# Optimization experiments

Hardware: AMD Instinct MI355X
Metric: run time of the kernel (lower is better)

Reference implementation:

```python
import jax, jax.numpy as jnp
import numpy as np

B, N, E, D = 8, 10000, 160000, 256
H = D // 2
SLOPE = 0.2  # LeakyReLU negative slope


def setup_inputs() -> dict:
    key = jax.random.key(0)
    ks = jax.random.split(key, 8)
    node_feats = jax.random.normal(ks[0], (B, N, D), dtype=jnp.float32)
    edge_attr = jax.random.uniform(ks[1], (E, 1), dtype=jnp.float32)
    W1 = jax.random.normal(ks[2], (2 * D, H), dtype=jnp.float32) * 0.05
    b1 = jnp.zeros((H,), dtype=jnp.float32)
    W2 = jax.random.normal(ks[3], (H, 1), dtype=jnp.float32) * 0.05
    b2 = jnp.zeros((1,), dtype=jnp.float32)
    edge_index = jax.random.randint(ks[4], (2, E), 0, N, dtype=jnp.int64)
    valid_masks = jax.random.randint(ks[5], (B, N), 0, 2).astype(bool)
    return {"node_feats": node_feats, "edge_attr": edge_attr, "W1": W1, "b1": b1,
            "W2": W2, "b2": b2, "edge_index": edge_index, "valid_masks": valid_masks}


def reference(node_feats, edge_attr, W1, b1, W2, b2, edge_index, valid_masks):
    # node_feats: [B,N,D]; edge_index: [2,E] shared across batch
    d = node_feats.shape[-1]
    src, dst = edge_index[0], edge_index[1]
    # cat([src_feats, dst_feats]) @ W1 == src @ W1[:d] + dst @ W1[d:]
    # Project per-node first, then gather per-edge: avoids the [B,E,2D] concat.
    ps = jnp.einsum('bnd,dh->bnh', node_feats, W1[:d])   # [B,N,H]
    pd = jnp.einsum('bnd,dh->bnh', node_feats, W1[d:])   # [B,N,H]
    h = ps[:, src] + pd[:, dst] + b1                      # [B,E,H]
    h = jnp.where(h >= 0, h, SLOPE * h)                   # LeakyReLU(0.2)
    scores = jnp.einsum('beh,h->be', h, W2[:, 0]) + b2[0]  # [B,E]
    scores = scores * edge_attr[:, 0]                     # edge_attr multiplies pre-softmax
    w = jax.nn.softmax(scores, axis=1)                    # global softmax over all edges
    # sparse_coo(edge_index, w) @ node_feats: out[src[e]] += w[e] * feats[dst[e]]
    msg = w[..., None] * node_feats[:, dst]               # [B,E,D]
    n = node_feats.shape[1]
    agg = jax.vmap(lambda m: jax.ops.segment_sum(m, src, num_segments=n))(msg)  # [B,N,D]
    mask = valid_masks.astype(node_feats.dtype)           # [B,N]
    cnt = mask.sum(axis=1)                                # [B]
    masked_mean = (agg * mask[..., None]).sum(axis=1) / jnp.maximum(cnt, 1.0)[:, None]
    full_mean = agg.mean(axis=1)
    graph_feats = jnp.where((cnt > 0)[:, None], masked_mean, full_mean)  # [B,D]
    return graph_feats, w
```

## Files before the change

### kernel.cpp

```cpp
#include <hip/hip_runtime.h>
#include <hip/hip_bf16.h>
#include <hip/hip_fp16.h>

#define B_ 8
#define N_ 10000
#define E_ 160000
#define D_ 256
#define H_ 128
#define SLOPE 0.2f
#define NCHUNK 100

#define NB_ 64
#define EPB_ (E_ / NB_)
#define BINS_ 256
#define NPB_ (N_ / 16)
#define SUBS_ 8

#define SB_ 256
#define SEB_ (E_ / SB_)

typedef __attribute__((ext_vector_type(8))) _Float16 v8h;
typedef __attribute__((ext_vector_type(4))) _Float16 v4h;
typedef __attribute__((ext_vector_type(2))) _Float16 v2h;
typedef __attribute__((ext_vector_type(4))) float f32x4;

static __device__ __forceinline__ float dot2f(v2h a, v2h b, float c) {
#if __has_builtin(__builtin_amdgcn_fdot2)
    return __builtin_amdgcn_fdot2(a, b, c, false);
#else
    return fmaf((float)a.y, (float)b.y, fmaf((float)a.x, (float)b.x, c));
#endif
}

static __device__ __forceinline__ void block_flags(const int* __restrict__ eidx_raw,
                                                   const unsigned int* __restrict__ mask32,
                                                   int tid, int* sfl) {
    if (tid < 64) {
        unsigned long long oddnz = __ballot(eidx_raw[2 * tid + 1] != 0);
        unsigned long long mgt1  = __ballot(mask32[tid] > 1u);
        if (tid == 0) {
            sfl[0] = (oddnz == 0ull) ? 1 : 0;
            sfl[1] = (mgt1 != 0ull) ? 1 : 0;
        }
    }
    __syncthreads();
}

__global__ __launch_bounds__(256) void kprep(const int* __restrict__ eidx_raw,
                                             const unsigned char* __restrict__ mask8,
                                             const unsigned int* __restrict__ mask32,
                                             const float* __restrict__ W1,
                                             const float* __restrict__ b1,
                                             const float* __restrict__ W2,
                                             int* __restrict__ ce,
                                             unsigned char* __restrict__ cmT,
                                             __half* __restrict__ Wt,
                                             __half* __restrict__ b1h,
                                             __half* __restrict__ w2h,
                                             int* __restrict__ cnti,
                                             int* __restrict__ hpart) {
    const int tid = threadIdx.x;
    __shared__ int sfl[2];
    __shared__ int scnt[8];

    if (blockIdx.x < 1250) {
        if (tid < 8) scnt[tid] = 0;
        block_flags(eidx_raw, mask32, tid, sfl);
        const int f_e = sfl[0], f_m = sfl[1];
        const int i = blockIdx.x * 256 + tid;
        if (i < 2 * E_) ce[i] = f_e ? eidx_raw[2 * i] : eidx_raw[i];
        if (i < B_ * N_) {
            unsigned char v = f_m ? (unsigned char)(mask8[i] != 0)
                                  : (unsigned char)(mask32[i] != 0u);
            const int b = i / N_;
            const int n = i - b * N_;
            cmT[n * 8 + b] = v;
            if (v) atomicAdd(&scnt[b], 1);
        }
        if (i < 2 * 256 * 128) {
            const int f = i & 127;
            const int row = i >> 7;
            const int c = row >> 8, k = row & 255;
            Wt[((c * 128 + f) * 256) + k] = __float2half(W1[row * 128 + f]);
        }
        if (i < 128) {
            b1h[i] = __float2half(b1[i]);
            w2h[i] = __float2half(W2[i]);
        }
        __syncthreads();
        if (tid < 8 && scnt[tid]) atomicAdd(&cnti[tid], scnt[tid]);
    } else {
        block_flags(eidx_raw, mask32, tid, sfl);
        const int f_e = sfl[0];
        __shared__ int h[BINS_];
        h[tid] = 0;
        __syncthreads();
        const int hb = blockIdx.x - 1250;
        const int base = hb * EPB_;
        for (int i = tid; i < EPB_; i += 256) {
            const int e = base + i;
            const int s = f_e ? eidx_raw[2 * e] : eidx_raw[e];
            const int d = f_e ? eidx_raw[2 * (E_ + e)] : eidx_raw[E_ + e];
            const int bin = (d / NPB_) * 16 + s / NPB_;
            atomicAdd(&h[bin], 1);
        }
        __syncthreads();
        hpart[hb * BINS_ + tid] = h[tid];
    }
}

__global__ __launch_bounds__(256) void kprefix(const int* __restrict__ hpart,
                                               int* __restrict__ offsetG,
                                               int* __restrict__ bstart) {
    __shared__ int cnt[BINS_];
    __shared__ int excl[BINS_];
    const int bin = threadIdx.x;
    int c = 0;
    for (int b = 0; b < NB_; b++) c += hpart[b * BINS_ + bin];
    cnt[bin] = c;
    __syncthreads();
    if (bin == 0) {
        int r = 0;
        for (int i = 0; i < BINS_; i++) { excl[i] = r; r += cnt[i]; }
    }
    __syncthreads();
    if ((bin & 15) == 0) bstart[bin >> 4] = excl[bin];
    if (bin == 0) bstart[16] = E_;
    int run = excl[bin];
    for (int b = 0; b < NB_; b++) {
        offsetG[b * BINS_ + bin] = run;
        run += hpart[b * BINS_ + bin];
    }
}

__global__ __launch_bounds__(256) void k1_mfma(const float* __restrict__ X,
                                               const __half* __restrict__ Wt,
                                               __half* __restrict__ ps,
                                               __half* __restrict__ pd,
                                               const int* __restrict__ ce,
                                               const int* __restrict__ offsetG,
                                               int4* __restrict__ esort,
                                               int* __restrict__ rank) {
    const int tid = threadIdx.x;
    __shared__ __align__(16) char smem[64 * 136 * 2];

    if (blockIdx.x >= 1250) {
        int* loc = (int*)smem;
        const int sb = blockIdx.x - 1250;
        loc[tid] = offsetG[sb * BINS_ + tid];
        __syncthreads();
        const int base = sb * EPB_;
        for (int i = tid; i < EPB_; i += 256) {
            const int e = base + i;
            const int s = ce[e], d = ce[E_ + e];
            const int bin = (d / NPB_) * 16 + s / NPB_;
            const int pos = atomicAdd(&loc[bin], 1);
            esort[pos] = make_int4(s, d, e, 0);
            rank[e] = pos;
        }
        return;
    }

    const int rb = blockIdx.x;
    const int wave = tid >> 6, lane = tid & 63;
    const int quad = lane >> 4, l16 = lane & 15;
    _Float16* Xs = (_Float16*)smem;
    _Float16* T  = (_Float16*)smem;

    f32x4 acc[2][2][4];
#pragma unroll
    for (int c = 0; c < 2; c++)
#pragma unroll
        for (int i = 0; i < 2; i++)
#pragma unroll
            for (int j = 0; j < 4; j++) acc[c][i][j] = (f32x4){0.f, 0.f, 0.f, 0.f};

    const int row_base = rb * 64;
    const int sr = tid >> 3;
    const int sc = (tid & 7) * 4;

    const float* xsrc  = &X[(size_t)(row_base + sr) * 256 + sc];
    const float* xsrc2 = xsrc + 32 * 256;
    const __half* wbase = &Wt[((size_t)(wave * 32 + l16)) * 256 + quad * 8];

    float4 xa, xb;
    v8h wcur[2][2], wnxt[2][2];

    xa = *(const float4*)(xsrc);
    xb = *(const float4*)(xsrc2);
#pragma unroll
    for (int cb = 0; cb < 2; cb++)
#pragma unroll
        for (int ft = 0; ft < 2; ft++)
            wcur[cb][ft] = *(const v8h*)(wbase + (size_t)(cb * 128 + ft * 16) * 256);
    {
        v4h pa = {(_Float16)xa.x, (_Float16)xa.y, (_Float16)xa.z, (_Float16)xa.w};
        v4h pb = {(_Float16)xb.x, (_Float16)xb.y, (_Float16)xb.z, (_Float16)xb.w};
        *(v4h*)&Xs[sr * 40 + sc] = pa;
        *(v4h*)&Xs[(sr + 32) * 40 + sc] = pb;
    }
    __syncthreads();

    for (int kc = 0; kc < 8; ++kc) {
        const int cur = kc & 1;
        if (kc < 7) {
            xa = *(const float4*)(xsrc + (kc + 1) * 32);
            xb = *(const float4*)(xsrc2 + (kc + 1) * 32);
#pragma unroll
            for (int cb = 0; cb < 2; cb++)
#pragma unroll
                for (int ft = 0; ft < 2; ft++)
                    wnxt[cb][ft] = *(const v8h*)(wbase + (size_t)(cb * 128 + ft * 16) * 256 + (kc + 1) * 32);
        }
#pragma unroll
        for (int nt = 0; nt < 4; ++nt) {
            v8h xf = *(v8h*)&Xs[cur * (64 * 40) + (nt * 16 + l16) * 40 + quad * 8];
            acc[0][0][nt] = __builtin_amdgcn_mfma_f32_16x16x32_f16(wcur[0][0], xf, acc[0][0][nt], 0, 0, 0);
            acc[0][1][nt] = __builtin_amdgcn_mfma_f32_16x16x32_f16(wcur[0][1], xf, acc[0][1][nt], 0, 0, 0);
            acc[1][0][nt] = __builtin_amdgcn_mfma_f32_16x16x32_f16(wcur[1][0], xf, acc[1][0][nt], 0, 0, 0);
            acc[1][1][nt] = __builtin_amdgcn_mfma_f32_16x16x32_f16(wcur[1][1], xf, acc[1][1][nt], 0, 0, 0);
        }
        if (kc < 7) {
            const int nb = (cur ^ 1) * (64 * 40);
            v4h pa = {(_Float16)xa.x, (_Float16)xa.y, (_Float16)xa.z, (_Float16)xa.w};
            v4h pb = {(_Float16)xb.x, (_Float16)xb.y, (_Float16)xb.z, (_Float16)xb.w};
            *(v4h*)&Xs[nb + sr * 40 + sc] = pa;
            *(v4h*)&Xs[nb + (sr + 32) * 40 + sc] = pb;
#pragma unroll
            for (int cb = 0; cb < 2; cb++)
#pragma unroll
                for (int ft = 0; ft < 2; ft++)
                    wcur[cb][ft] = wnxt[cb][ft];
        }
        __syncthreads();
    }

#pragma unroll
    for (int cb = 0; cb < 2; ++cb) {
        if (cb) __syncthreads();
#pragma unroll
        for (int nt = 0; nt < 4; ++nt)
#pragma unroll
            for (int ft = 0; ft < 2; ++ft) {
                f32x4 a = acc[cb][ft][nt];
                v4h h = {(_Float16)a.x, (_Float16)a.y, (_Float16)a.z, (_Float16)a.w};
                *(v4h*)&T[(nt * 16 + l16) * 136 + wave * 32 + ft * 16 + quad * 4] = h;
            }
        __syncthreads();
        __half* outp = cb ? pd : ps;
#pragma unroll
        for (int pass = 0; pass < 4; ++pass) {
            const int r = pass * 16 + (tid >> 4);
            const int f8 = (tid & 15) * 8;
            const int R = row_base + r;
            const int b = R / N_;
            const int n = R - b * N_;
            *(float4*)(outp + ((size_t)b * N_ + n) * 128 + f8) =
                *(const float4*)&T[r * 136 + f8];
        }
    }
}

__global__ __launch_bounds__(256) void k2_scores(const __half* __restrict__ ps,
                                                 const __half* __restrict__ pd,
                                                 const int4* __restrict__ esort,
                                                 const __half* __restrict__ b1h,
                                                 const __half* __restrict__ w2h,
                                                 const float* __restrict__ b2,
                                                 const float* __restrict__ eattr,
                                                 float* __restrict__ scS) {
    const int tid = threadIdx.x;
    const int wave = tid >> 6;
    const int lane = tid & 63;
    const int bid = blockIdx.x;
    const int batch = bid & 7;
    const int e0 = (bid >> 3) * 64;

    const int hi = (lane & 7) * 16;

    v2h b1p[8], w2p[8];
    {
        const v2h* bp = (const v2h*)(b1h + hi);
        const v2h* wp = (const v2h*)(w2h + hi);
#pragma unroll
        for (int j = 0; j < 8; j++) { b1p[j] = bp[j]; w2p[j] = wp[j]; }
    }
    const float bias2 = b2[0];
    const v2h slp = {(_Float16)SLOPE, (_Float16)SLOPE};

    const __half* psb = ps + (size_t)batch * N_ * 128;
    const __half* pdb = pd + (size_t)batch * N_ * 128;
    float* scb = scS + (size_t)batch * E_;

#pragma unroll
    for (int q = 0; q < 2; q++) {
        const int e = e0 + wave * 16 + q * 8 + (lane >> 3);
        const int4 er = esort[e];
        const int src = er.x, dst = er.y, orig = er.z;

        const float4* aps = (const float4*)&psb[(size_t)src * 128 + hi];
        const float4* apd = (const float4*)&pdb[(size_t)dst * 128 + hi];
        float4 rs[2] = {aps[0], aps[1]};
        float4 rd[2] = {apd[0], apd[1]};
        const v2h* sv = (const v2h*)rs;
        const v2h* dv = (const v2h*)rd;

        float acc = 0.f;
#pragma unroll
        for (int j = 0; j < 8; j++) {
            v2h x = sv[j] + dv[j] + b1p[j];
            v2h l = __builtin_elementwise_max(x, x * slp);
            acc = dot2f(l, w2p[j], acc);
        }
        acc += __shfl_xor(acc, 1);
        acc += __shfl_xor(acc, 2);
        acc += __shfl_xor(acc, 4);

        if ((lane & 7) == 0) {
            scb[e] = (acc + bias2) * eattr[orig];
        }
    }
}

__global__ __launch_bounds__(256) void k3s_stats(const float* __restrict__ scS,
                                                 float* __restrict__ pmax,
                                                 double* __restrict__ psum) {
    const int tid = threadIdx.x;
    const int wave = tid >> 6, lane = tid & 63;
    const int base = blockIdx.x * SEB_;

    float fm[8];
#pragma unroll
    for (int j = 0; j < 8; j++) fm[j] = -3.4e38f;
    for (int i = tid; i < SEB_; i += 256) {
        const int p = base + i;
#pragma unroll
        for (int j = 0; j < 8; j++)
            fm[j] = fmaxf(fm[j], scS[(size_t)j * E_ + p]);
    }
#pragma unroll
    for (int k = 1; k <= 32; k <<= 1)
#pragma unroll
        for (int j = 0; j < 8; j++) fm[j] = fmaxf(fm[j], __shfl_xor(fm[j], k));
    __shared__ float lmax[4][8];
    if (lane == 0)
#pragma unroll
        for (int j = 0; j < 8; j++) lmax[wave][j] = fm[j];
    __syncthreads();
    float m[8];
#pragma unroll
    for (int j = 0; j < 8; j++)
        m[j] = fmaxf(fmaxf(lmax[0][j], lmax[1][j]), fmaxf(lmax[2][j], lmax[3][j]));

    double s[8];
#pragma unroll
    for (int j = 0; j < 8; j++) s[j] = 0.0;
    for (int i = tid; i < SEB_; i += 256) {
        const int p = base + i;
#pragma unroll
        for (int j = 0; j < 8; j++)
            s[j] += (double)expf(scS[(size_t)j * E_ + p] - m[j]);
    }
#pragma unroll
    for (int k = 1; k <= 32; k <<= 1)
#pragma unroll
        for (int j = 0; j < 8; j++) s[j] += __shfl_xor(s[j], k);
    __shared__ double lsum[4][8];
    if (lane == 0)
#pragma unroll
        for (int j = 0; j < 8; j++) lsum[wave][j] = s[j];
    __syncthreads();
    if (tid < 8) {
        pmax[blockIdx.x * 8 + tid] = m[tid];
        psum[blockIdx.x * 8 + tid] = lsum[0][tid] + lsum[1][tid] + lsum[2][tid] + lsum[3][tid];
    }
}

static __device__ __forceinline__ void stats_combine(const float* __restrict__ pmax,
                                                     const double* __restrict__ psum,
                                                     int tid, float* smx, float* sinvx) {
    if (tid < 64) {
        float mc[SB_ / 64][8];
        float v[8];
#pragma unroll
        for (int j = 0; j < 8; j++) v[j] = -3.4e38f;
#pragma unroll
        for (int g = 0; g < SB_ / 64; g++) {
            const float4* p4 = (const float4*)&pmax[(g * 64 + tid) * 8];
            float4 a = p4[0], b = p4[1];
            mc[g][0] = a.x; mc[g][1] = a.y; mc[g][2] = a.z; mc[g][3] = a.w;
            mc[g][4] = b.x; mc[g][5] = b.y; mc[g][6] = b.z; mc[g][7] = b.w;
#pragma unroll
            for (int j = 0; j < 8; j++) v[j] = fmaxf(v[j], mc[g][j]);
        }
#pragma unroll
        for (int k = 1; k <= 32; k <<= 1)
#pragma unroll
            for (int j = 0; j < 8; j++) v[j] = fmaxf(v[j], __shfl_xor(v[j], k));
        double z[8];
#pragma unroll
        for (int j = 0; j < 8; j++) z[j] = 0.0;
#pragma unroll
        for (int g = 0; g < SB_ / 64; g++)
#pragma unroll
            for (int j = 0; j < 8; j++)
                z[j] += psum[(g * 64 + tid) * 8 + j] * (double)expf(mc[g][j] - v[j]);
#pragma unroll
        for (int k = 1; k <= 32; k <<= 1)
#pragma unroll
            for (int j = 0; j < 8; j++) z[j] += __shfl_xor(z[j], k);
        if (tid == 0)
#pragma unroll
            for (int j = 0; j < 8; j++) { smx[j] = v[j]; sinvx[j] = (float)(1.0 / z[j]); }
    }
}

__global__ __launch_bounds__(256) void k3ef(const int4* __restrict__ esort,
                                            const float* __restrict__ scS,
                                            const unsigned char* __restrict__ cmT,
                                            const float* __restrict__ pmax,
                                            const double* __restrict__ psum,
                                            const int* __restrict__ bstart,
                                            const int* __restrict__ rank,
                                            float* __restrict__ Wpf,
                                            float* __restrict__ Wpm,
                                            float* __restrict__ wout) {
    const int tid = threadIdx.x;
    __shared__ float smx[8], sinvx[8];
    __shared__ float lWf[NPB_ * 8];
    __shared__ float lWm[NPB_ * 8];

    stats_combine(pmax, psum, tid, smx, sinvx);

    if (blockIdx.x >= 16 * SUBS_) {
        __syncthreads();
        const int e = (blockIdx.x - 16 * SUBS_) * 256 + tid;
        const int p = rank[e];
#pragma unroll
        for (int j = 0; j < 8; j++) {
            const float v = scS[(size_t)j * E_ + p];
            wout[(size_t)j * E_ + e] = expf(v - smx[j]) * sinvx[j];
        }
        return;
    }

    const int bucket = blockIdx.x / SUBS_;
    const int sub = blockIdx.x % SUBS_;

    for (int i = tid; i < NPB_ * 8; i += 256) { lWf[i] = 0.f; lWm[i] = 0.f; }
    __syncthreads();

    float m[8], inv[8];
#pragma unroll
    for (int j = 0; j < 8; j++) { m[j] = smx[j]; inv[j] = sinvx[j]; }

    const int bs = bstart[bucket], be = bstart[bucket + 1];
    const int len = be - bs;
    const int s0 = bs + (int)((long long)len * sub / SUBS_);
    const int s1 = bs + (int)((long long)len * (sub + 1) / SUBS_);
    const int nbase = bucket * NPB_;

    for (int p = s0 + tid; p < s1; p += 256) {
        const int4 er = esort[p];
        const int src = er.x;
        const int rel = er.y - nbase;
        float wv[8];
#pragma unroll
        for (int j = 0; j < 8; j++)
            wv[j] = expf(scS[(size_t)j * E_ + p] - m[j]) * inv[j];
        const unsigned long long mm = *(const unsigned long long*)&cmT[src * 8];
        float* lf = &lWf[rel * 8];
        float* lm = &lWm[rel * 8];
#pragma unroll
        for (int j = 0; j < 8; j++) {
            atomicAdd(&lf[j], wv[j]);
            if ((mm >> (8 * j)) & 1ull) atomicAdd(&lm[j], wv[j]);
        }
    }
    __syncthreads();

    float* of = Wpf + ((size_t)bucket * SUBS_ + sub) * (NPB_ * 8);
    float* om = Wpm + ((size_t)bucket * SUBS_ + sub) * (NPB_ * 8);
    for (int i = tid; i < NPB_ * 8; i += 256) { of[i] = lWf[i]; om[i] = lWm[i]; }
}

__global__ __launch_bounds__(256) void k3g_reduce(const float* __restrict__ Wpf,
                                                  const float* __restrict__ Wpm,
                                                  float* __restrict__ WfT,
                                                  float* __restrict__ WmT) {
    const int i = blockIdx.x * 256 + threadIdx.x;
    if (i >= N_ * 8) return;
    const int n = i >> 3, b = i & 7;
    const int bucket = n / NPB_;
    const int rel = n - bucket * NPB_;
    float sf = 0.f, sm = 0.f;
#pragma unroll
    for (int sub = 0; sub < SUBS_; sub++) {
        const size_t off = ((size_t)bucket * SUBS_ + sub) * (NPB_ * 8) + rel * 8 + b;
        sf += Wpf[off];
        sm += Wpm[off];
    }
    WfT[i] = sf;
    WmT[i] = sm;
}

__global__ __launch_bounds__(256) void k4b_wsum(const float* __restrict__ X,
                                                const float* __restrict__ WmT,
                                                const float* __restrict__ WfT,
                                                float* __restrict__ gpart) {
    const int c = blockIdx.x;
    const int b = blockIdx.y;
    const int tx = threadIdx.x & 63;
    const int ty = threadIdx.x >> 6;
    const int npc = N_ / NCHUNK;
    const int n0 = c * npc;

    const float4* X4 = (const float4*)(X + (size_t)b * N_ * 256);
    float4 am = {0.f, 0.f, 0.f, 0.f};
    float4 af = {0.f, 0.f, 0.f, 0.f};

    for (int n = n0 + ty; n < n0 + npc; n += 4) {
        float wm = WmT[n * 8 + b];
        float wf = WfT[n * 8 + b];
        float4 v = X4[(size_t)n * 64 + tx];
        am.x = fmaf(wm, v.x, am.x); am.y = fmaf(wm, v.y, am.y);
        am.z = fmaf(wm, v.z, am.z); am.w = fmaf(wm, v.w, am.w);
        af.x = fmaf(wf, v.x, af.x); af.y = fmaf(wf, v.y, af.y);
        af.z = fmaf(wf, v.z, af.z); af.w = fmaf(wf, v.w, af.w);
    }

    __shared__ float4 red[256];
    red[threadIdx.x] = am;
    __syncthreads();
    if (ty == 0) {
        float4 r1 = red[tx + 64], r2 = red[tx + 128], r3 = red[tx + 192];
        am.x += r1.x + r2.x + r3.x; am.y += r1.y + r2.y + r3.y;
        am.z += r1.z + r2.z + r3.z; am.w += r1.w + r2.w + r3.w;
    }
    __syncthreads();
    red[threadIdx.x] = af;
    __syncthreads();
    if (ty == 0) {
        float4 r1 = red[tx + 64], r2 = red[tx + 128], r3 = red[tx + 192];
        af.x += r1.x + r2.x + r3.x; af.y += r1.y + r2.y + r3.y;
        af.z += r1.z + r2.z + r3.z; af.w += r1.w + r2.w + r3.w;
        float4* gp4 = (float4*)gpart;
        gp4[((c * 2 + 0) * 8 + b) * 64 + tx] = am;
        gp4[((c * 2 + 1) * 8 + b) * 64 + tx] = af;
    }
}

__global__ __launch_bounds__(256) void k5_final(const float* __restrict__ gpart,
                                                const int* __restrict__ cnti,
                                                float* __restrict__ gf) {
    const int b = blockIdx.x;
    const int d = threadIdx.x;
    float sm = 0.f, sf = 0.f;
    for (int c = 0; c < NCHUNK; c++) {
        sm += gpart[((c * 2 + 0) * 8 + b) * 256 + d];
        sf += gpart[((c * 2 + 1) * 8 + b) * 256 + d];
    }
    const float cn = (float)cnti[b];
    gf[b * 256 + d] = (cn > 0.f) ? (sm / cn) : (sf / (float)N_);
}

static inline char* align16(char* p) {
    return (char*)(((uintptr_t)p + 15) & ~(uintptr_t)15);
}

extern "C" void kernel_launch(void* const* d_in, const int* in_sizes, int n_in,
                              void* d_out, int out_size, void* d_ws, size_t ws_size,
                              hipStream_t stream) {
    const float* X     = (const float*)d_in[0];
    const float* eattr = (const float*)d_in[1];
    const float* W1    = (const float*)d_in[2];
    const float* b1    = (const float*)d_in[3];
    const float* W2    = (const float*)d_in[4];
    const float* b2    = (const float*)d_in[5];
    const int*   eidx_raw = (const int*)d_in[6];
    const unsigned char* mask8 = (const unsigned char*)d_in[7];
    const unsigned int*  mask32 = (const unsigned int*)d_in[7];

    float* out  = (float*)d_out;
    float* gf   = out;
    float* wout = out + 2048;

    char* cur = (char*)d_ws;
    __half* ps_h = (__half*)cur;             cur += (size_t)N_ * 8 * 128 * 2;
    __half* pd_h = (__half*)cur;             cur += (size_t)N_ * 8 * 128 * 2;
    __half* Wt   = (__half*)cur;             cur += 2 * 128 * 256 * 2;
    int* ce      = (int*)cur;                cur += 2 * E_ * 4;
    unsigned char* cmT = (unsigned char*)cur; cur += N_ * 8;
    cur = align16(cur);
    int* cnti    = (int*)cur;                cur += 8 * 4;
    cur = align16(cur);
    float* pmax  = (float*)cur;              cur += SB_ * 8 * 4;
    cur = align16(cur);
    double* psum = (double*)cur;             cur += SB_ * 8 * 8;
    float* gpart = (float*)cur;              cur += NCHUNK * 2 * 8 * 256 * 4;
    int* hpart   = (int*)cur;                cur += NB_ * BINS_ * 4;
    int* offsetG = (int*)cur;                cur += NB_ * BINS_ * 4;
    int* bstart  = (int*)cur;                cur += 32 * 4;
    cur = align16(cur);
    int4* esort  = (int4*)cur;               cur += (size_t)E_ * 16;
    int* rankB   = (int*)cur;                cur += E_ * 4;
    __half* b1h  = (__half*)cur;             cur += 128 * 2;
    __half* w2h  = (__half*)cur;             cur += 128 * 2;
    cur = align16(cur);
    float* scS   = (float*)cur;              cur += (size_t)E_ * 8 * 4;

    char* ocur = (char*)d_ws;
    float* Wpf = (float*)ocur;               ocur += (size_t)16 * SUBS_ * NPB_ * 8 * 4;
    float* Wpm = (float*)ocur;               ocur += (size_t)16 * SUBS_ * NPB_ * 8 * 4;
    float* WfT = (float*)ocur;               ocur += N_ * 8 * 4;
    float* WmT = (float*)ocur;               ocur += N_ * 8 * 4;

    hipMemsetAsync(cnti, 0, 8 * sizeof(int), stream);
    hipLaunchKernelGGL(kprep, dim3(1250 + NB_), dim3(256), 0, stream,
                       eidx_raw, mask8, mask32, W1, b1, W2,
                       ce, cmT, Wt, b1h, w2h, cnti, hpart);
    hipLaunchKernelGGL(kprefix, dim3(1), dim3(256), 0, stream, hpart, offsetG, bstart);
    hipLaunchKernelGGL(k1_mfma, dim3(1250 + NB_), dim3(256), 0, stream,
                       X, Wt, ps_h, pd_h, ce, offsetG, esort, rankB);
    hipLaunchKernelGGL(k2_scores, dim3(E_ / 8), dim3(256), 0, stream,
                       ps_h, pd_h, esort, b1h, w2h, b2, eattr, scS);
    hipLaunchKernelGGL(k3s_stats, dim3(SB_), dim3(256), 0, stream, scS, pmax, psum);
    hipLaunchKernelGGL(k3ef, dim3(16 * SUBS_ + E_ / 256), dim3(256), 0, stream,
                       esort, scS, cmT, pmax, psum, bstart, rankB, Wpf, Wpm, wout);
    hipLaunchKernelGGL(k3g_reduce, dim3((N_ * 8 + 255) / 256), dim3(256), 0, stream,
                       Wpf, Wpm, WfT, WmT);
    hipLaunchKernelGGL(k4b_wsum, dim3(NCHUNK, 8), dim3(256), 0, stream, X, WmT, WfT, gpart);
    hipLaunchKernelGGL(k5_final, dim3(8), dim3(256), 0, stream, gpart, cnti, gf);
}
```

Measured before the change: 276.6 us.

## Fuse prefix scan, sub-bucket reduce and final reduce into neighbouring kernels

Moves the histogram prefix scan into block 0 of the projection kernel, with the scatter blocks spinning on a release/acquire flag. Folds the per-sub-bucket weight reduction into the weighted-sum kernel, and replaces the final reduction kernel with global atomics plus a last-block ticket that writes the output. This removes three kernel launches and their intermediate buffers. It adds spin-wait dependencies on block scheduling order, float atomics that make the output order-nondeterministic, and eight-fold redundant loads of the partial weights per row.

```diff
diff --git a/kernel.cpp b/kernel.cpp
--- a/kernel.cpp
+++ b/kernel.cpp
@@ -58,7 +58,10 @@
                                              __half* __restrict__ b1h,
                                              __half* __restrict__ w2h,
                                              int* __restrict__ cnti,
-                                             int* __restrict__ hpart) {
+                                             int* __restrict__ hpart,
+                                             int* __restrict__ flagp,
+                                             int* __restrict__ ticketp,
+                                             float* __restrict__ gaccum) {
     const int tid = threadIdx.x;
     __shared__ int sfl[2];
     __shared__ int scnt[8];
@@ -96,6 +99,10 @@
         h[tid] = 0;
         __syncthreads();
         const int hb = blockIdx.x - 1250;
+        if (hb == 0) {
+            if (tid == 0) { flagp[0] = 0; ticketp[0] = 0; }
+            for (int i = tid; i < 4096; i += 256) gaccum[i] = 0.f;
+        }
         const int base = hb * EPB_;
         for (int i = tid; i < EPB_; i += 256) {
             const int e = base + i;
@@ -109,44 +116,55 @@
     }
 }
 
-__global__ __launch_bounds__(256) void kprefix(const int* __restrict__ hpart,
-                                               int* __restrict__ offsetG,
-                                               int* __restrict__ bstart) {
-    __shared__ int cnt[BINS_];
-    __shared__ int excl[BINS_];
-    const int bin = threadIdx.x;
-    int c = 0;
-    for (int b = 0; b < NB_; b++) c += hpart[b * BINS_ + bin];
-    cnt[bin] = c;
-    __syncthreads();
-    if (bin == 0) {
-        int r = 0;
-        for (int i = 0; i < BINS_; i++) { excl[i] = r; r += cnt[i]; }
-    }
-    __syncthreads();
-    if ((bin & 15) == 0) bstart[bin >> 4] = excl[bin];
-    if (bin == 0) bstart[16] = E_;
-    int run = excl[bin];
-    for (int b = 0; b < NB_; b++) {
-        offsetG[b * BINS_ + bin] = run;
-        run += hpart[b * BINS_ + bin];
-    }
-}
-
 __global__ __launch_bounds__(256) void k1_mfma(const float* __restrict__ X,
                                                const __half* __restrict__ Wt,
                                                __half* __restrict__ ps,
                                                __half* __restrict__ pd,
                                                const int* __restrict__ ce,
-                                               const int* __restrict__ offsetG,
+                                               const int* __restrict__ hpart,
+                                               int* __restrict__ offsetG,
+                                               int* __restrict__ bstart,
+                                               int* __restrict__ flagp,
                                                int4* __restrict__ esort,
                                                int* __restrict__ rank) {
     const int tid = threadIdx.x;
     __shared__ __align__(16) char smem[64 * 136 * 2];
 
-    if (blockIdx.x >= 1250) {
+    if (blockIdx.x == 0) {
+        int* cnt  = (int*)smem;
+        int* excl = (int*)smem + BINS_;
+        const int bin = tid;
+        int c = 0;
+        for (int b = 0; b < NB_; b++) c += hpart[b * BINS_ + bin];
+        cnt[bin] = c;
+        __syncthreads();
+        if (bin == 0) {
+            int r = 0;
+            for (int i = 0; i < BINS_; i++) { excl[i] = r; r += cnt[i]; }
+        }
+        __syncthreads();
+        if ((bin & 15) == 0) bstart[bin >> 4] = excl[bin];
+        if (bin == 0) bstart[16] = E_;
+        int run = excl[bin];
+        for (int b = 0; b < NB_; b++) {
+            offsetG[b * BINS_ + bin] = run;
+            run += hpart[b * BINS_ + bin];
+        }
+        __threadfence();
+        __syncthreads();
+        if (tid == 0)
+            __hip_atomic_store(flagp, 1, __ATOMIC_RELEASE, __HIP_MEMORY_SCOPE_AGENT);
+        return;
+    }
+
+    if (blockIdx.x <= NB_) {
+        if (tid == 0) {
+            while (__hip_atomic_load(flagp, __ATOMIC_ACQUIRE, __HIP_MEMORY_SCOPE_AGENT) == 0)
+                __builtin_amdgcn_s_sleep(2);
+        }
+        __syncthreads();
         int* loc = (int*)smem;
-        const int sb = blockIdx.x - 1250;
+        const int sb = blockIdx.x - 1;
         loc[tid] = offsetG[sb * BINS_ + tid];
         __syncthreads();
         const int base = sb * EPB_;
@@ -161,7 +179,7 @@
         return;
     }
 
-    const int rb = blockIdx.x;
+    const int rb = blockIdx.x - (NB_ + 1);
     const int wave = tid >> 6, lane = tid & 63;
     const int quad = lane >> 4, l16 = lane & 15;
     _Float16* Xs = (_Float16*)smem;
@@ -484,30 +502,13 @@
     for (int i = tid; i < NPB_ * 8; i += 256) { of[i] = lWf[i]; om[i] = lWm[i]; }
 }
 
-__global__ __launch_bounds__(256) void k3g_reduce(const float* __restrict__ Wpf,
-                                                  const float* __restrict__ Wpm,
-                                                  float* __restrict__ WfT,
-                                                  float* __restrict__ WmT) {
-    const int i = blockIdx.x * 256 + threadIdx.x;
-    if (i >= N_ * 8) return;
-    const int n = i >> 3, b = i & 7;
-    const int bucket = n / NPB_;
-    const int rel = n - bucket * NPB_;
-    float sf = 0.f, sm = 0.f;
-#pragma unroll
-    for (int sub = 0; sub < SUBS_; sub++) {
-        const size_t off = ((size_t)bucket * SUBS_ + sub) * (NPB_ * 8) + rel * 8 + b;
-        sf += Wpf[off];
-        sm += Wpm[off];
-    }
-    WfT[i] = sf;
-    WmT[i] = sm;
-}
-
 __global__ __launch_bounds__(256) void k4b_wsum(const float* __restrict__ X,
-                                                const float* __restrict__ WmT,
-                                                const float* __restrict__ WfT,
-                                                float* __restrict__ gpart) {
+                                                const float* __restrict__ Wpf,
+                                                const float* __restrict__ Wpm,
+                                                const int* __restrict__ cnti,
+                                                float* __restrict__ gaccum,
+                                                int* __restrict__ ticketp,
+                                                float* __restrict__ gf) {
     const int c = blockIdx.x;
     const int b = blockIdx.y;
     const int tx = threadIdx.x & 63;
@@ -520,8 +521,15 @@
     float4 af = {0.f, 0.f, 0.f, 0.f};
 
     for (int n = n0 + ty; n < n0 + npc; n += 4) {
-        float wm = WmT[n * 8 + b];
-        float wf = WfT[n * 8 + b];
+        const int bucket = n / NPB_;
+        const int rel = n - bucket * NPB_;
+        float wm = 0.f, wf = 0.f;
+#pragma unroll
+        for (int sub = 0; sub < SUBS_; sub++) {
+            const size_t off = ((size_t)bucket * SUBS_ + sub) * (NPB_ * 8) + rel * 8 + b;
+            wf += Wpf[off];
+            wm += Wpm[off];
+        }
         float4 v = X4[(size_t)n * 64 + tx];
         am.x = fmaf(wm, v.x, am.x); am.y = fmaf(wm, v.y, am.y);
         am.z = fmaf(wm, v.z, am.z); am.w = fmaf(wm, v.w, am.w);
@@ -544,24 +552,30 @@
         float4 r1 = red[tx + 64], r2 = red[tx + 128], r3 = red[tx + 192];
         af.x += r1.x + r2.x + r3.x; af.y += r1.y + r2.y + r3.y;
         af.z += r1.z + r2.z + r3.z; af.w += r1.w + r2.w + r3.w;
-        float4* gp4 = (float4*)gpart;
-        gp4[((c * 2 + 0) * 8 + b) * 64 + tx] = am;
-        gp4[((c * 2 + 1) * 8 + b) * 64 + tx] = af;
-    }
-}
-
-__global__ __launch_bounds__(256) void k5_final(const float* __restrict__ gpart,
-                                                const int* __restrict__ cnti,
-                                                float* __restrict__ gf) {
-    const int b = blockIdx.x;
-    const int d = threadIdx.x;
-    float sm = 0.f, sf = 0.f;
-    for (int c = 0; c < NCHUNK; c++) {
-        sm += gpart[((c * 2 + 0) * 8 + b) * 256 + d];
-        sf += gpart[((c * 2 + 1) * 8 + b) * 256 + d];
-    }
-    const float cn = (float)cnti[b];
-    gf[b * 256 + d] = (cn > 0.f) ? (sm / cn) : (sf / (float)N_);
+        float* ga0 = gaccum + b * 256 + tx * 4;
+        float* ga1 = gaccum + 2048 + b * 256 + tx * 4;
+        atomicAdd(ga0 + 0, am.x); atomicAdd(ga0 + 1, am.y);
+        atomicAdd(ga0 + 2, am.z); atomicAdd(ga0 + 3, am.w);
+        atomicAdd(ga1 + 0, af.x); atomicAdd(ga1 + 1, af.y);
+        atomicAdd(ga1 + 2, af.z); atomicAdd(ga1 + 3, af.w);
+    }
+
+    __threadfence();
+    __syncthreads();
+    __shared__ int sdone;
+    if (threadIdx.x == 0) sdone = atomicAdd(ticketp, 1);
+    __syncthreads();
+    if (sdone == NCHUNK * 8 - 1) {
+        for (int i = threadIdx.x; i < 2048; i += 256) {
+            const int bb = i >> 8, d = i & 255;
+            const float sm = __hip_atomic_load(&gaccum[bb * 256 + d],
+                                               __ATOMIC_RELAXED, __HIP_MEMORY_SCOPE_AGENT);
+            const float sf = __hip_atomic_load(&gaccum[2048 + bb * 256 + d],
+                                               __ATOMIC_RELAXED, __HIP_MEMORY_SCOPE_AGENT);
+            const float cn = (float)cnti[bb];
+            gf[bb * 256 + d] = (cn > 0.f) ? (sm / cn) : (sf / (float)N_);
+        }
+    }
 }
 
 static inline char* align16(char* p) {
@@ -593,11 +607,14 @@
     unsigned char* cmT = (unsigned char*)cur; cur += N_ * 8;
     cur = align16(cur);
     int* cnti    = (int*)cur;                cur += 8 * 4;
+    int* flagp   = (int*)cur;                cur += 4;
+    int* ticketp = (int*)cur;                cur += 4;
+    cur = align16(cur);
+    float* gaccum = (float*)cur;             cur += 4096 * 4;
     cur = align16(cur);
     float* pmax  = (float*)cur;              cur += SB_ * 8 * 4;
     cur = align16(cur);
     double* psum = (double*)cur;             cur += SB_ * 8 * 8;
-    float* gpart = (float*)cur;              cur += NCHUNK * 2 * 8 * 256 * 4;
     int* hpart   = (int*)cur;                cur += NB_ * BINS_ * 4;
     int* offsetG = (int*)cur;                cur += NB_ * BINS_ * 4;
     int* bstart  = (int*)cur;                cur += 32 * 4;
@@ -612,23 +629,18 @@
     char* ocur = (char*)d_ws;
     float* Wpf = (float*)ocur;               ocur += (size_t)16 * SUBS_ * NPB_ * 8 * 4;
     float* Wpm = (float*)ocur;               ocur += (size_t)16 * SUBS_ * NPB_ * 8 * 4;
-    float* WfT = (float*)ocur;               ocur += N_ * 8 * 4;
-    float* WmT = (float*)ocur;               ocur += N_ * 8 * 4;
 
     hipMemsetAsync(cnti, 0, 8 * sizeof(int), stream);
     hipLaunchKernelGGL(kprep, dim3(1250 + NB_), dim3(256), 0, stream,
                        eidx_raw, mask8, mask32, W1, b1, W2,
-                       ce, cmT, Wt, b1h, w2h, cnti, hpart);
-    hipLaunchKernelGGL(kprefix, dim3(1), dim3(256), 0, stream, hpart, offsetG, bstart);
-    hipLaunchKernelGGL(k1_mfma, dim3(1250 + NB_), dim3(256), 0, stream,
-                       X, Wt, ps_h, pd_h, ce, offsetG, esort, rankB);
+                       ce, cmT, Wt, b1h, w2h, cnti, hpart, flagp, ticketp, gaccum);
+    hipLaunchKernelGGL(k1_mfma, dim3(1 + NB_ + 1250), dim3(256), 0, stream,
+                       X, Wt, ps_h, pd_h, ce, hpart, offsetG, bstart, flagp, esort, rankB);
     hipLaunchKernelGGL(k2_scores, dim3(E_ / 8), dim3(256), 0, stream,
                        ps_h, pd_h, esort, b1h, w2h, b2, eattr, scS);
     hipLaunchKernelGGL(k3s_stats, dim3(SB_), dim3(256), 0, stream, scS, pmax, psum);
     hipLaunchKernelGGL(k3ef, dim3(16 * SUBS_ + E_ / 256), dim3(256), 0, stream,
                        esort, scS, cmT, pmax, psum, bstart, rankB, Wpf, Wpm, wout);
-    hipLaunchKernelGGL(k3g_reduce, dim3((N_ * 8 + 255) / 256), dim3(256), 0, stream,
-                       Wpf, Wpm, WfT, WmT);
-    hipLaunchKernelGGL(k4b_wsum, dim3(NCHUNK, 8), dim3(256), 0, stream, X, WmT, WfT, gpart);
-    hipLaunchKernelGGL(k5_final, dim3(8), dim3(256), 0, stream, gpart, cnti, gf);
-}
+    hipLaunchKernelGGL(k4b_wsum, dim3(NCHUNK, 8), dim3(256), 0, stream,
+                       X, Wpf, Wpm, cnti, gaccum, ticketp, gf);
+}
```

Measured after the change: 344.0 us. 24.4% more time.

## Fold prefix-scan kernel into projection kernel with flag-based inter-block sync

Applied to the files above, without the earlier changes.

Removes the separate single-block kprefix launch. Block 0 of k1_mfma now computes the bin prefix sums and publishes offsets through a release-store flag. The scatter blocks spin on an acquire-load until the flag is set, and the MFMA projection blocks run concurrently. This drops a kernel launch and its serialization gap. It relies on block 0 being scheduled before or alongside the spinning blocks, which is a forward-progress assumption.

```diff
diff --git a/kernel.cpp b/kernel.cpp
--- a/kernel.cpp
+++ b/kernel.cpp
@@ -58,7 +58,8 @@
                                              __half* __restrict__ b1h,
                                              __half* __restrict__ w2h,
                                              int* __restrict__ cnti,
-                                             int* __restrict__ hpart) {
+                                             int* __restrict__ hpart,
+                                             int* __restrict__ flagp) {
     const int tid = threadIdx.x;
     __shared__ int sfl[2];
     __shared__ int scnt[8];
@@ -96,6 +97,7 @@
         h[tid] = 0;
         __syncthreads();
         const int hb = blockIdx.x - 1250;
+        if (hb == 0 && tid == 0) flagp[0] = 0;
         const int base = hb * EPB_;
         for (int i = tid; i < EPB_; i += 256) {
             const int e = base + i;
@@ -109,44 +111,55 @@
     }
 }
 
-__global__ __launch_bounds__(256) void kprefix(const int* __restrict__ hpart,
-                                               int* __restrict__ offsetG,
-                                               int* __restrict__ bstart) {
-    __shared__ int cnt[BINS_];
-    __shared__ int excl[BINS_];
-    const int bin = threadIdx.x;
-    int c = 0;
-    for (int b = 0; b < NB_; b++) c += hpart[b * BINS_ + bin];
-    cnt[bin] = c;
-    __syncthreads();
-    if (bin == 0) {
-        int r = 0;
-        for (int i = 0; i < BINS_; i++) { excl[i] = r; r += cnt[i]; }
-    }
-    __syncthreads();
-    if ((bin & 15) == 0) bstart[bin >> 4] = excl[bin];
-    if (bin == 0) bstart[16] = E_;
-    int run = excl[bin];
-    for (int b = 0; b < NB_; b++) {
-        offsetG[b * BINS_ + bin] = run;
-        run += hpart[b * BINS_ + bin];
-    }
-}
-
 __global__ __launch_bounds__(256) void k1_mfma(const float* __restrict__ X,
                                                const __half* __restrict__ Wt,
                                                __half* __restrict__ ps,
                                                __half* __restrict__ pd,
                                                const int* __restrict__ ce,
-                                               const int* __restrict__ offsetG,
+                                               const int* __restrict__ hpart,
+                                               int* __restrict__ offsetG,
+                                               int* __restrict__ bstart,
+                                               int* __restrict__ flagp,
                                                int4* __restrict__ esort,
                                                int* __restrict__ rank) {
     const int tid = threadIdx.x;
     __shared__ __align__(16) char smem[64 * 136 * 2];
 
-    if (blockIdx.x >= 1250) {
+    if (blockIdx.x == 0) {
+        int* cnt  = (int*)smem;
+        int* excl = (int*)smem + BINS_;
+        const int bin = tid;
+        int c = 0;
+        for (int b = 0; b < NB_; b++) c += hpart[b * BINS_ + bin];
+        cnt[bin] = c;
+        __syncthreads();
+        if (bin == 0) {
+            int r = 0;
+            for (int i = 0; i < BINS_; i++) { excl[i] = r; r += cnt[i]; }
+        }
+        __syncthreads();
+        if ((bin & 15) == 0) bstart[bin >> 4] = excl[bin];
+        if (bin == 0) bstart[16] = E_;
+        int run = excl[bin];
+        for (int b = 0; b < NB_; b++) {
+            offsetG[b * BINS_ + bin] = run;
+            run += hpart[b * BINS_ + bin];
+        }
+        __threadfence();
+        __syncthreads();
+        if (tid == 0)
+            __hip_atomic_store(flagp, 1, __ATOMIC_RELEASE, __HIP_MEMORY_SCOPE_AGENT);
+        return;
+    }
+
+    if (blockIdx.x <= NB_) {
+        if (tid == 0) {
+            while (__hip_atomic_load(flagp, __ATOMIC_ACQUIRE, __HIP_MEMORY_SCOPE_AGENT) == 0)
+                __builtin_amdgcn_s_sleep(2);
+        }
+        __syncthreads();
         int* loc = (int*)smem;
-        const int sb = blockIdx.x - 1250;
+        const int sb = blockIdx.x - 1;
         loc[tid] = offsetG[sb * BINS_ + tid];
         __syncthreads();
         const int base = sb * EPB_;
@@ -161,7 +174,7 @@
         return;
     }
 
-    const int rb = blockIdx.x;
+    const int rb = blockIdx.x - (NB_ + 1);
     const int wave = tid >> 6, lane = tid & 63;
     const int quad = lane >> 4, l16 = lane & 15;
     _Float16* Xs = (_Float16*)smem;
@@ -593,6 +606,7 @@
     unsigned char* cmT = (unsigned char*)cur; cur += N_ * 8;
     cur = align16(cur);
     int* cnti    = (int*)cur;                cur += 8 * 4;
+    int* flagp   = (int*)cur;                cur += 4;
     cur = align16(cur);
     float* pmax  = (float*)cur;              cur += SB_ * 8 * 4;
     cur = align16(cur);
@@ -618,10 +632,9 @@
     hipMemsetAsync(cnti, 0, 8 * sizeof(int), stream);
     hipLaunchKernelGGL(kprep, dim3(1250 + NB_), dim3(256), 0, stream,
                        eidx_raw, mask8, mask32, W1, b1, W2,
-                       ce, cmT, Wt, b1h, w2h, cnti, hpart);
-    hipLaunchKernelGGL(kprefix, dim3(1), dim3(256), 0, stream, hpart, offsetG, bstart);
-    hipLaunchKernelGGL(k1_mfma, dim3(1250 + NB_), dim3(256), 0, stream,
-                       X, Wt, ps_h, pd_h, ce, offsetG, esort, rankB);
+                       ce, cmT, Wt, b1h, w2h, cnti, hpart, flagp);
+    hipLaunchKernelGGL(k1_mfma, dim3(1 + NB_ + 1250), dim3(256), 0, stream,
+                       X, Wt, ps_h, pd_h, ce, hpart, offsetG, bstart, flagp, esort, rankB);
     hipLaunchKernelGGL(k2_scores, dim3(E_ / 8), dim3(256), 0, stream,
                        ps_h, pd_h, esort, b1h, w2h, b2, eattr, scS);
     hipLaunchKernelGGL(k3s_stats, dim3(SB_), dim3(256), 0, stream, scS, pmax, psum);
```

Measured after the change: 276.3 us. About the same (-0.1%).
